# Kernel tuning notes

Hardware: AMD Instinct MI355X
Metric: run time of the kernel (lower is better)

## Reference

```python
import jax, jax.numpy as jnp
import numpy as np

B, T, C = 8, 2048, 1024  # batch, seq_len (== block_size), n_embed
HEAD = 64


def setup_inputs() -> dict:
    key = jax.random.key(0)
    k1, k2, k3, k4 = jax.random.split(key, 4)
    x = jax.random.normal(k1, (B, T, C), dtype=jnp.float32)
    # nn.Linear(n_embed, head_size, bias=False) -> weight [head, C]; stored as [C, head]
    Wk = jax.random.normal(k2, (C, HEAD), dtype=jnp.float32) * (C ** -0.5)
    Wq = jax.random.normal(k3, (C, HEAD), dtype=jnp.float32) * (C ** -0.5)
    Wv = jax.random.normal(k4, (C, HEAD), dtype=jnp.float32) * (C ** -0.5)
    return {"x": x, "Wk": Wk, "Wq": Wq, "Wv": Wv}


def reference(x, Wk, Wq, Wv):
    Bx, Tx, Cx = x.shape
    k = jnp.einsum('btc,ch->bth', x, Wk)  # [B,T,HEAD]
    q = jnp.einsum('btc,ch->bth', x, Wq)
    v = jnp.einsum('btc,ch->bth', x, Wv)
    # Source quirk: scores = k @ q^T (k rows), scaled by n_embed**-0.5 (C, not head_size)
    scores = jnp.einsum('bih,bjh->bij', k, q) * (Cx ** -0.5)  # [B,T,T]
    causal = jnp.tril(jnp.ones((Tx, Tx), dtype=bool))
    scores = jnp.where(causal, scores, -jnp.inf)
    attn = jax.nn.softmax(scores, axis=-1)
    out = jnp.einsum('bij,bjh->bih', attn, v)  # [B,T,HEAD]
    return out
```

## Files before the change

### kernel.cpp

```cpp
#include <hip/hip_runtime.h>
#include <cstdint>

#define B_ 8
#define T_ 2048
#define C_ 1024
#define H_ 64
#define BT_ (B_ * T_)

typedef short short8 __attribute__((ext_vector_type(8)));
typedef short bh4 __attribute__((ext_vector_type(4)));
typedef float f32x4 __attribute__((ext_vector_type(4)));

__device__ inline short f2bf(float f) {
  uint32_t u = __float_as_uint(f);
  u += 0x7fffu + ((u >> 16) & 1u);
  return (short)(u >> 16);
}

__device__ __forceinline__ void gl_lds16(const void* g, void* l) {
  __builtin_amdgcn_global_load_lds(
      (const __attribute__((address_space(1))) unsigned int*)g,
      (__attribute__((address_space(3))) unsigned int*)l, 16, 0, 0);
}

__global__ __launch_bounds__(256) void prep_w(
    const float* __restrict__ Wk, const float* __restrict__ Wq,
    const float* __restrict__ Wv, short* __restrict__ Wt) {
  __shared__ float wl[64][68];
  const int mat = blockIdx.x >> 4;
  const int kc = blockIdx.x & 15;
  const float* W = (mat == 0) ? Wk : (mat == 1) ? Wq : Wv;
  const float sc = (mat == 0) ? 0.03125f * 1.44269504088896f : 1.0f;
  const int t = threadIdx.x;
  const int k0 = kc * 64;
#pragma unroll
  for (int j = 0; j < 4; ++j) {
    int s = t + 256 * j;
    int kr = s >> 4, cf = s & 15;
    float4 v = *reinterpret_cast<const float4*>(&W[(size_t)(k0 + kr) * H_ + cf * 4]);
    wl[kr][cf * 4 + 0] = v.x; wl[kr][cf * 4 + 1] = v.y;
    wl[kr][cf * 4 + 2] = v.z; wl[kr][cf * 4 + 3] = v.w;
  }
  __syncthreads();
#pragma unroll
  for (int j = 0; j < 2; ++j) {
    int s = t + 256 * j;
    int n = s >> 3, g = s & 7;
    short8 o;
#pragma unroll
    for (int i = 0; i < 8; ++i) o[i] = f2bf(wl[8 * g + i][n] * sc);
    *reinterpret_cast<short8*>(&Wt[(size_t)(mat * 64 + n) * C_ + k0 + 8 * g]) = o;
  }
}

__global__ __launch_bounds__(256, 1) void proj_kernel(
    const float* __restrict__ x, const short* __restrict__ Wt,
    short* __restrict__ Kp, short* __restrict__ Qp, short* __restrict__ Vt) {
  __shared__ float xs[2][32 * 64];
  __shared__ short ws[2][192 * 64];
  const int t = threadIdx.x;
  const int w = t >> 6, lane = t & 63;
  const int l15 = lane & 15, lg = lane >> 4;
  const int rg = w >> 1, ch = w & 1;
  const int rowBase = blockIdx.x * 32;

  f32x4 acc[6];
  const f32x4 zf = {0.f, 0.f, 0.f, 0.f};
#pragma unroll
  for (int i = 0; i < 6; ++i) acc[i] = zf;

  auto stage = [&](int buf, int k0) {
#pragma unroll
    for (int j = 0; j < 2; ++j) {
      const int seg = w * 2 + j;
      const int r = seg * 4 + (lane >> 4);
      const float* g =
          &x[(size_t)(rowBase + r) * C_ + k0 + (((lane & 15) ^ (r & 7)) << 2)];
      gl_lds16(g, (char*)&xs[buf][0] + seg * 1024);
    }
#pragma unroll
    for (int j = 0; j < 6; ++j) {
      const int seg = w * 6 + j;
      const int n = seg * 8 + (lane >> 3);
      const short* g =
          &Wt[(size_t)n * C_ + k0 + (((lane & 7) ^ (n & 7)) << 3)];
      gl_lds16(g, (char*)&ws[buf][0] + seg * 1024);
    }
  };

  stage(0, 0);

#pragma unroll 1
  for (int it = 0; it < 16; ++it) {
    __syncthreads();
    const int cb = it & 1;
    if (it < 15) stage(cb ^ 1, (it + 1) * 64);
    const int arow = 16 * rg + l15;
    const int x7 = arow & 7;
    const float* xrow = &xs[cb][arow * 64];
    float4 fa = *reinterpret_cast<const float4*>(xrow + (((2 * lg) ^ x7) << 2));
    float4 fb = *reinterpret_cast<const float4*>(xrow + (((2 * lg + 1) ^ x7) << 2));
    float4 fc = *reinterpret_cast<const float4*>(xrow + (((2 * lg + 8) ^ x7) << 2));
    float4 fd = *reinterpret_cast<const float4*>(xrow + (((2 * lg + 9) ^ x7) << 2));
    short8 a0, a1;
    a0[0] = f2bf(fa.x); a0[1] = f2bf(fa.y); a0[2] = f2bf(fa.z); a0[3] = f2bf(fa.w);
    a0[4] = f2bf(fb.x); a0[5] = f2bf(fb.y); a0[6] = f2bf(fb.z); a0[7] = f2bf(fb.w);
    a1[0] = f2bf(fc.x); a1[1] = f2bf(fc.y); a1[2] = f2bf(fc.z); a1[3] = f2bf(fc.w);
    a1[4] = f2bf(fd.x); a1[5] = f2bf(fd.y); a1[6] = f2bf(fd.z); a1[7] = f2bf(fd.w);
#pragma unroll
    for (int nt = 0; nt < 6; ++nt) {
      const int n2 = 16 * (6 * ch + nt) + l15, n7 = n2 & 7;
      const short* wrow = &ws[cb][n2 * 64];
      short8 b0 = *reinterpret_cast<const short8*>(wrow + ((lg ^ n7) << 3));
      short8 b1 = *reinterpret_cast<const short8*>(wrow + (((4 + lg) ^ n7) << 3));
      acc[nt] = __builtin_amdgcn_mfma_f32_16x16x32_bf16(a0, b0, acc[nt], 0, 0, 0);
      acc[nt] = __builtin_amdgcn_mfma_f32_16x16x32_bf16(a1, b1, acc[nt], 0, 0, 0);
    }
  }

  const int strip = blockIdx.x * 2 + rg;
  const int rb = strip * 16;
#pragma unroll
  for (int nt = 0; nt < 6; ++nt) {
    const int ntg = 6 * ch + nt;
    if (ntg < 8) {
      short* O = (ntg < 4) ? Kp : Qp;
      const int col = (ntg & 3) * 16 + l15;
#pragma unroll
      for (int r = 0; r < 4; ++r)
        O[(size_t)(rb + lg * 4 + r) * H_ + col] = f2bf(acc[nt][r]);
    }
  }
  __syncthreads();
  if (ch == 1) {
    short* vl = reinterpret_cast<short*>(&xs[0][0]) + rg * (16 * 66);
#pragma unroll
    for (int nt = 2; nt < 6; ++nt)
#pragma unroll
      for (int r = 0; r < 4; ++r)
        vl[(lg * 4 + r) * 66 + (nt - 2) * 16 + l15] = f2bf(acc[nt][r]);
    asm volatile("s_waitcnt lgkmcnt(0)" ::: "memory");
    short8 o0, o1;
#pragma unroll
    for (int i = 0; i < 8; ++i) o0[i] = vl[i * 66 + lane];
#pragma unroll
    for (int i = 0; i < 8; ++i) o1[i] = vl[(8 + i) * 66 + lane];
    const int bb = strip >> 7, tb = (strip & 127) * 16;
    short* dst = &Vt[((size_t)bb * H_ + lane) * T_ + tb];
    *reinterpret_cast<short8*>(dst) = o0;
    *reinterpret_cast<short8*>(dst + 8) = o1;
  }
}

__global__ __launch_bounds__(256) void attn_kernel(
    const short* __restrict__ Kq, const short* __restrict__ Qk,
    const short* __restrict__ Vt, float* __restrict__ out) {
  __shared__ short Ks[4][64 * 64];
  __shared__ short Vs[4][64 * 64];
  const int t = threadIdx.x, w = t >> 6, lane = t & 63;
  const int l15 = lane & 15, lg = lane >> 4;
  const int batch = blockIdx.x & 7;
  const int g = blockIdx.x >> 3;
  const int s = (g < 32) ? (63 - g) : (g - 32);
  const int p = w & 1;
  const int rg = w >> 1;
  const short* Kb = Kq + (size_t)batch * T_ * H_;
  const short* Qb = Qk + (size_t)batch * T_ * H_;
  const short* Vb = Vt + (size_t)batch * H_ * T_;
  float* ob = out + (size_t)batch * T_ * H_;
  const f32x4 zf = {0.f, 0.f, 0.f, 0.f};
  const int k7 = l15 & 7;

  const int qbase = s * 32;
  const int qrow = qbase + rg * 16 + l15;
  const short8 qa0 = *reinterpret_cast<const short8*>(&Kb[(size_t)qrow * H_ + lg * 8]);
  const short8 qa1 = *reinterpret_cast<const short8*>(&Kb[(size_t)qrow * H_ + lg * 8 + 32]);
  const int nkt = (s >> 1) + 1;
  const int np = (nkt + 1) >> 1;

  const int srow = lane >> 3;
  const int ssw = ((lane & 7) ^ srow) << 3;
  auto stage = [&](int per) {
    const int tj = 2 * per + (w >> 1);
    if (tj >= nkt) return;
    const int buf = (per & 1) * 2 + (w >> 1);
    const int kbase = tj * 64;
    const int h4 = (w & 1) * 4;
#pragma unroll
    for (int g2 = 0; g2 < 4; ++g2) {
      const int gg = h4 + g2;
      gl_lds16(&Qb[(size_t)(kbase + gg * 8 + srow) * H_ + ssw],
               (char*)&Ks[buf][0] + gg * 1024);
      gl_lds16(&Vb[(size_t)(gg * 8 + srow) * T_ + kbase + ssw],
               (char*)&Vs[buf][0] + gg * 1024);
    }
  };

  f32x4 O[4];
#pragma unroll
  for (int i = 0; i < 4; ++i) O[i] = zf;
  float m = -1e30f, l = 0.f;

  stage(0);

#pragma unroll 1
  for (int j = 0; j < np; ++j) {
    __syncthreads();
    if (j + 1 < np) stage(j + 1);
    const int kt = 2 * j + p;
    if (kt < nkt) {
      const int cb = (j & 1) * 2 + p;
      const int kbase = kt * 64;
      f32x4 S[4];
      __builtin_amdgcn_s_setprio(1);
#pragma unroll
      for (int nt = 0; nt < 4; ++nt) {
        S[nt] = zf;
        const short* krow = &Ks[cb][(16 * nt + l15) * 64];
        short8 kf0 = *reinterpret_cast<const short8*>(&krow[(lg ^ k7) << 3]);
        short8 kf1 = *reinterpret_cast<const short8*>(&krow[((4 + lg) ^ k7) << 3]);
        S[nt] = __builtin_amdgcn_mfma_f32_16x16x32_bf16(kf0, qa0, S[nt], 0, 0, 0);
        S[nt] = __builtin_amdgcn_mfma_f32_16x16x32_bf16(kf1, qa1, S[nt], 0, 0, 0);
      }
      __builtin_amdgcn_s_setprio(0);
      if (kt == nkt - 1) {
#pragma unroll
        for (int nt = 0; nt < 4; ++nt) {
          const int klo = kbase + 16 * nt + 4 * lg;
#pragma unroll
          for (int r = 0; r < 4; ++r)
            if (klo + r > qrow) S[nt][r] = -1e30f;
        }
      }
      float mx0 = fmaxf(fmaxf(S[0][0], S[0][1]), fmaxf(S[0][2], S[0][3]));
      float mx1 = fmaxf(fmaxf(S[1][0], S[1][1]), fmaxf(S[1][2], S[1][3]));
      float mx2 = fmaxf(fmaxf(S[2][0], S[2][1]), fmaxf(S[2][2], S[2][3]));
      float mx3 = fmaxf(fmaxf(S[3][0], S[3][1]), fmaxf(S[3][2], S[3][3]));
      float mx = fmaxf(fmaxf(mx0, mx1), fmaxf(mx2, mx3));
      mx = fmaxf(mx, __shfl_xor(mx, 16));
      mx = fmaxf(mx, __shfl_xor(mx, 32));
      const float mn = fmaxf(m, mx);
      const float scv = exp2f(m - mn);
      m = mn;
      float rs = 0.f;
#pragma unroll
      for (int nt = 0; nt < 4; ++nt)
#pragma unroll
        for (int r = 0; r < 4; ++r) {
          const float pv = exp2f(S[nt][r] - mn);
          S[nt][r] = pv;
          rs += pv;
        }
      rs += __shfl_xor(rs, 16);
      rs += __shfl_xor(rs, 32);
      l = l * scv + rs;
#pragma unroll
      for (int nt = 0; nt < 4; ++nt) O[nt] *= scv;
      const int d7 = l15 & 7;
      const int vo = 4 * (lg & 1);
      __builtin_amdgcn_s_setprio(1);
#pragma unroll
      for (int kc = 0; kc < 2; ++kc) {
        short8 pa;
#pragma unroll
        for (int jj = 0; jj < 8; ++jj)
          pa[jj] = f2bf(S[2 * kc + (jj >> 2)][jj & 3]);
        const int slo = ((4 * kc + (lg >> 1)) ^ d7) << 3;
        const int shi = ((4 * kc + 2 + (lg >> 1)) ^ d7) << 3;
#pragma unroll
        for (int nt = 0; nt < 4; ++nt) {
          const short* vrow = &Vs[cb][(16 * nt + l15) * 64];
          const bh4 vlo = *reinterpret_cast<const bh4*>(&vrow[slo + vo]);
          const bh4 vhi = *reinterpret_cast<const bh4*>(&vrow[shi + vo]);
          short8 vf;
          vf[0] = vlo[0]; vf[1] = vlo[1]; vf[2] = vlo[2]; vf[3] = vlo[3];
          vf[4] = vhi[0]; vf[5] = vhi[1]; vf[6] = vhi[2]; vf[7] = vhi[3];
          O[nt] = __builtin_amdgcn_mfma_f32_16x16x32_bf16(vf, pa, O[nt], 0, 0, 0);
        }
      }
      __builtin_amdgcn_s_setprio(0);
    }
  }

  __syncthreads();
  float* Po = reinterpret_cast<float*>(&Ks[0][0]);
  float* Mlp = reinterpret_cast<float*>(&Vs[0][0]);
#pragma unroll
  for (int nt = 0; nt < 4; ++nt)
    *reinterpret_cast<f32x4*>(&Po[(w * 16 + l15) * 68 + 16 * nt + 4 * lg]) = O[nt];
  if (lane < 16) {
    Mlp[(w * 16 + l15) * 2 + 0] = m;
    Mlp[(w * 16 + l15) * 2 + 1] = l;
  }
  __syncthreads();
  {
    const int row = t >> 4, c4 = t & 15;
#pragma unroll
    for (int gg = 0; gg < 2; ++gg) {
      const int s0 = gg * 2, s1 = gg * 2 + 1;
      const float m0 = Mlp[(s0 * 16 + row) * 2], l0 = Mlp[(s0 * 16 + row) * 2 + 1];
      const float m1 = Mlp[(s1 * 16 + row) * 2], l1 = Mlp[(s1 * 16 + row) * 2 + 1];
      const float M = fmaxf(m0, m1);
      const float e0 = exp2f(m0 - M), e1 = exp2f(m1 - M);
      const float L = l0 * e0 + l1 * e1;
      const f32x4 o0 = *reinterpret_cast<const f32x4*>(&Po[(s0 * 16 + row) * 68 + c4 * 4]);
      const f32x4 o1 = *reinterpret_cast<const f32x4*>(&Po[(s1 * 16 + row) * 68 + c4 * 4]);
      const f32x4 res = (o0 * e0 + o1 * e1) * (1.f / L);
      *reinterpret_cast<f32x4*>(&ob[(size_t)(qbase + gg * 16 + row) * H_ + c4 * 4]) = res;
    }
  }
}

extern "C" void kernel_launch(void* const* d_in, const int* in_sizes, int n_in,
                              void* d_out, int out_size, void* d_ws, size_t ws_size,
                              hipStream_t stream) {
  const float* x = (const float*)d_in[0];
  const float* Wk = (const float*)d_in[1];
  const float* Wq = (const float*)d_in[2];
  const float* Wv = (const float*)d_in[3];
  float* out = (float*)d_out;

  short* Kp = (short*)d_ws;
  short* Qp = Kp + (size_t)BT_ * H_;
  short* Vt = Qp + (size_t)BT_ * H_;
  short* Wt = Vt + (size_t)BT_ * H_;

  hipLaunchKernelGGL(prep_w, dim3(48), dim3(256), 0, stream, Wk, Wq, Wv, Wt);
  hipLaunchKernelGGL(proj_kernel, dim3(512), dim3(256), 0, stream, x, Wt, Kp, Qp, Vt);
  hipLaunchKernelGGL(attn_kernel, dim3(512), dim3(256), 0, stream, Kp, Qp, Vt, out);
}
```

Baseline: 60.01 us.

## Split attention KV range across two blocks per 64-row strip and add combine kernel

The attention kernel now gives each block 64 query rows with 512 threads, and splits each strip's key tiles between two blocks by tile parity (even/odd). Each block writes an unnormalized partial output plus its max and sum to workspace. A new combine kernel merges the two partials into the final output. This is meant to balance causal work across blocks and raise per-block parallelism. The cost is an extra launch and an extra round trip of partial results through global memory.

After: 54.23 us. -9.6%, faster.

```diff
diff --git a/kernel.cpp b/kernel.cpp
--- a/kernel.cpp
+++ b/kernel.cpp
@@ -152,47 +152,56 @@
   }
 }
 
-__global__ __launch_bounds__(256) void attn_kernel(
+__global__ __launch_bounds__(512) void attn_kernel(
     const short* __restrict__ Kq, const short* __restrict__ Qk,
-    const short* __restrict__ Vt, float* __restrict__ out) {
+    const short* __restrict__ Vt, float* __restrict__ Pg,
+    float* __restrict__ Mg) {
   __shared__ short Ks[4][64 * 64];
   __shared__ short Vs[4][64 * 64];
   const int t = threadIdx.x, w = t >> 6, lane = t & 63;
   const int l15 = lane & 15, lg = lane >> 4;
   const int batch = blockIdx.x & 7;
-  const int g = blockIdx.x >> 3;
-  const int s = (g < 32) ? (63 - g) : (g - 32);
-  const int p = w & 1;
-  const int rg = w >> 1;
+  const int q = blockIdx.x >> 3;
+  const int sidx = (q < 32) ? (31 - q) : (q - 32);
+  const int h = (q < 32) ? 0 : 1;
+  const int p = w & 1, rg = w >> 1;
   const short* Kb = Kq + (size_t)batch * T_ * H_;
   const short* Qb = Qk + (size_t)batch * T_ * H_;
   const short* Vb = Vt + (size_t)batch * H_ * T_;
-  float* ob = out + (size_t)batch * T_ * H_;
   const f32x4 zf = {0.f, 0.f, 0.f, 0.f};
   const int k7 = l15 & 7;
 
-  const int qbase = s * 32;
+  const int qbase = sidx * 64;
   const int qrow = qbase + rg * 16 + l15;
   const short8 qa0 = *reinterpret_cast<const short8*>(&Kb[(size_t)qrow * H_ + lg * 8]);
   const short8 qa1 = *reinterpret_cast<const short8*>(&Kb[(size_t)qrow * H_ + lg * 8 + 32]);
-  const int nkt = (s >> 1) + 1;
-  const int np = (nkt + 1) >> 1;
-
+  const int ntiles = sidx + 1;
+  const int nlist = (h == 0) ? ((ntiles + 1) >> 1) : (ntiles >> 1);
+  const int np = (nlist + 1) >> 1;
+
+  const int tp = w >> 2, kind = (w >> 1) & 1, q2 = w & 1;
   const int srow = lane >> 3;
   const int ssw = ((lane & 7) ^ srow) << 3;
   auto stage = [&](int per) {
-    const int tj = 2 * per + (w >> 1);
-    if (tj >= nkt) return;
-    const int buf = (per & 1) * 2 + (w >> 1);
-    const int kbase = tj * 64;
-    const int h4 = (w & 1) * 4;
-#pragma unroll
-    for (int g2 = 0; g2 < 4; ++g2) {
-      const int gg = h4 + g2;
-      gl_lds16(&Qb[(size_t)(kbase + gg * 8 + srow) * H_ + ssw],
-               (char*)&Ks[buf][0] + gg * 1024);
-      gl_lds16(&Vb[(size_t)(gg * 8 + srow) * T_ + kbase + ssw],
-               (char*)&Vs[buf][0] + gg * 1024);
+    const int le = 2 * per + tp;
+    if (le >= nlist) return;
+    const int gkt = 2 * le + h;
+    const int buf = (per & 1) * 2 + tp;
+    const int kbase = gkt * 64;
+    if (kind == 0) {
+#pragma unroll
+      for (int g2 = 0; g2 < 4; ++g2) {
+        const int gg = q2 * 4 + g2;
+        gl_lds16(&Qb[(size_t)(kbase + gg * 8 + srow) * H_ + ssw],
+                 (char*)&Ks[buf][0] + gg * 1024);
+      }
+    } else {
+#pragma unroll
+      for (int g2 = 0; g2 < 4; ++g2) {
+        const int gg = q2 * 4 + g2;
+        gl_lds16(&Vb[(size_t)(gg * 8 + srow) * T_ + kbase + ssw],
+                 (char*)&Vs[buf][0] + gg * 1024);
+      }
     }
   };
 
@@ -204,13 +213,14 @@
   stage(0);
 
 #pragma unroll 1
-  for (int j = 0; j < np; ++j) {
+  for (int i = 0; i < np; ++i) {
     __syncthreads();
-    if (j + 1 < np) stage(j + 1);
-    const int kt = 2 * j + p;
-    if (kt < nkt) {
-      const int cb = (j & 1) * 2 + p;
-      const int kbase = kt * 64;
+    if (i + 1 < np) stage(i + 1);
+    const int le = 2 * i + p;
+    if (le < nlist) {
+      const int gkt = 2 * le + h;
+      const int cb = (i & 1) * 2 + p;
+      const int kbase = gkt * 64;
       f32x4 S[4];
       __builtin_amdgcn_s_setprio(1);
 #pragma unroll
@@ -223,7 +233,7 @@
         S[nt] = __builtin_amdgcn_mfma_f32_16x16x32_bf16(kf1, qa1, S[nt], 0, 0, 0);
       }
       __builtin_amdgcn_s_setprio(0);
-      if (kt == nkt - 1) {
+      if (gkt == sidx) {
 #pragma unroll
         for (int nt = 0; nt < 4; ++nt) {
           const int klo = kbase + 16 * nt + 4 * lg;
@@ -287,27 +297,55 @@
   float* Mlp = reinterpret_cast<float*>(&Vs[0][0]);
 #pragma unroll
   for (int nt = 0; nt < 4; ++nt)
-    *reinterpret_cast<f32x4*>(&Po[(w * 16 + l15) * 68 + 16 * nt + 4 * lg]) = O[nt];
+    *reinterpret_cast<f32x4*>(&Po[(w * 16 + l15) * 64 + 16 * nt + 4 * lg]) = O[nt];
   if (lane < 16) {
     Mlp[(w * 16 + l15) * 2 + 0] = m;
     Mlp[(w * 16 + l15) * 2 + 1] = l;
   }
   __syncthreads();
   {
-    const int row = t >> 4, c4 = t & 15;
-#pragma unroll
-    for (int gg = 0; gg < 2; ++gg) {
-      const int s0 = gg * 2, s1 = gg * 2 + 1;
-      const float m0 = Mlp[(s0 * 16 + row) * 2], l0 = Mlp[(s0 * 16 + row) * 2 + 1];
-      const float m1 = Mlp[(s1 * 16 + row) * 2], l1 = Mlp[(s1 * 16 + row) * 2 + 1];
+    const int c4 = t & 15;
+#pragma unroll
+    for (int hh = 0; hh < 2; ++hh) {
+      const int lr = (t >> 4) + 32 * hh;
+      const int w0 = (lr >> 4) * 2, w1 = w0 + 1;
+      const int r = lr & 15;
+      const float m0 = Mlp[(w0 * 16 + r) * 2], l0 = Mlp[(w0 * 16 + r) * 2 + 1];
+      const float m1 = Mlp[(w1 * 16 + r) * 2], l1 = Mlp[(w1 * 16 + r) * 2 + 1];
       const float M = fmaxf(m0, m1);
       const float e0 = exp2f(m0 - M), e1 = exp2f(m1 - M);
       const float L = l0 * e0 + l1 * e1;
-      const f32x4 o0 = *reinterpret_cast<const f32x4*>(&Po[(s0 * 16 + row) * 68 + c4 * 4]);
-      const f32x4 o1 = *reinterpret_cast<const f32x4*>(&Po[(s1 * 16 + row) * 68 + c4 * 4]);
-      const f32x4 res = (o0 * e0 + o1 * e1) * (1.f / L);
-      *reinterpret_cast<f32x4*>(&ob[(size_t)(qbase + gg * 16 + row) * H_ + c4 * 4]) = res;
-    }
+      const f32x4 o0 = *reinterpret_cast<const f32x4*>(&Po[(w0 * 16 + r) * 64 + c4 * 4]);
+      const f32x4 o1 = *reinterpret_cast<const f32x4*>(&Po[(w1 * 16 + r) * 64 + c4 * 4]);
+      const f32x4 om = o0 * e0 + o1 * e1;
+      const size_t gr = (size_t)batch * T_ + qbase + lr;
+      *reinterpret_cast<f32x4*>(&Pg[((size_t)h * BT_ + gr) * H_ + c4 * 4]) = om;
+      if (c4 == 0) {
+        Mg[((size_t)h * BT_ + gr) * 2 + 0] = M;
+        Mg[((size_t)h * BT_ + gr) * 2 + 1] = L;
+      }
+    }
+  }
+}
+
+__global__ __launch_bounds__(256) void combine_kernel(
+    const float* __restrict__ Pg, const float* __restrict__ Mg,
+    float* __restrict__ out) {
+  const int t = threadIdx.x;
+#pragma unroll
+  for (int k = 0; k < 2; ++k) {
+    const int task = blockIdx.x * 512 + k * 256 + t;
+    const int row = task >> 4;
+    const int c4 = task & 15;
+    const float M0 = Mg[(size_t)row * 2], L0 = Mg[(size_t)row * 2 + 1];
+    const float M1 = Mg[((size_t)BT_ + row) * 2], L1 = Mg[((size_t)BT_ + row) * 2 + 1];
+    const float M = fmaxf(M0, M1);
+    const float e0 = exp2f(M0 - M), e1 = exp2f(M1 - M);
+    const float L = L0 * e0 + L1 * e1;
+    const f32x4 o0 = *reinterpret_cast<const f32x4*>(&Pg[(size_t)row * H_ + c4 * 4]);
+    const f32x4 o1 = *reinterpret_cast<const f32x4*>(&Pg[((size_t)BT_ + row) * H_ + c4 * 4]);
+    const f32x4 res = (o0 * e0 + o1 * e1) * (1.f / L);
+    *reinterpret_cast<f32x4*>(&out[(size_t)row * H_ + c4 * 4]) = res;
   }
 }
 
@@ -324,8 +362,11 @@
   short* Qp = Kp + (size_t)BT_ * H_;
   short* Vt = Qp + (size_t)BT_ * H_;
   short* Wt = Vt + (size_t)BT_ * H_;
+  float* Pg = (float*)(Wt + 192 * C_);
+  float* Mg = Pg + (size_t)2 * BT_ * H_;
 
   hipLaunchKernelGGL(prep_w, dim3(48), dim3(256), 0, stream, Wk, Wq, Wv, Wt);
   hipLaunchKernelGGL(proj_kernel, dim3(512), dim3(256), 0, stream, x, Wt, Kp, Qp, Vt);
-  hipLaunchKernelGGL(attn_kernel, dim3(512), dim3(256), 0, stream, Kp, Qp, Vt, out);
-}
+  hipLaunchKernelGGL(attn_kernel, dim3(512), dim3(512), 0, stream, Kp, Qp, Vt, Pg, Mg);
+  hipLaunchKernelGGL(combine_kernel, dim3(512), dim3(256), 0, stream, Pg, Mg, out);
+}
```
